# Kernel optimization log

Measured on AMD Instinct MI355X. Metric: run time of the kernel, lower is better.

Reference implementation:

```python
import jax, jax.numpy as jnp
import numpy as np

N = 50000      # nodes
E = 1600000    # edges (before self-loops)
H = 4          # heads
C = 32         # channels per head
HC = H * C     # hidden_channels = 128
IN = 128       # in_channels
NCLS = 4       # classifier out_channels
B = 512        # number of graphs
NEG_SLOPE = 0.2


def setup_inputs() -> dict:
    key = jax.random.key(0)
    ks = jax.random.split(key, 14)
    s = 0.1
    return {
        "x": jax.random.normal(ks[0], (N, IN), jnp.float32),
        "edge_index": jax.random.randint(ks[1], (2, E), 0, N, dtype=jnp.int32),
        "batch": jnp.sort(jax.random.randint(ks[2], (N,), 0, B, dtype=jnp.int32)),
        "w1": jax.random.normal(ks[3], (IN, HC), jnp.float32) * s,
        "as1": jax.random.normal(ks[4], (H, C), jnp.float32) * s,
        "ad1": jax.random.normal(ks[5], (H, C), jnp.float32) * s,
        "b1": jnp.zeros((HC,), jnp.float32),
        "w2": jax.random.normal(ks[6], (HC, HC), jnp.float32) * s,
        "as2": jax.random.normal(ks[7], (H, C), jnp.float32) * s,
        "ad2": jax.random.normal(ks[8], (H, C), jnp.float32) * s,
        "b2": jnp.zeros((HC,), jnp.float32),
        "wc": jax.random.normal(ks[9], (HC, NCLS), jnp.float32) * s,
        "bc": jnp.zeros((NCLS,), jnp.float32),
    }


def gat_conv(x, W, a_src, a_dst, bias, src, dst):
    # x: [N, F_in]; W: [F_in, H*C]
    h = (x @ W).reshape(N, H, C)                      # [N, H, C]
    e_src = jnp.einsum('nhc,hc->nh', h, a_src)        # [N, H]
    e_dst = jnp.einsum('nhc,hc->nh', h, a_dst)
    # per-edge attention logits, softmax grouped by destination node
    e = jax.nn.leaky_relu(e_src[src] + e_dst[dst], NEG_SLOPE)      # [E', H]
    m = jax.ops.segment_max(e, dst, num_segments=N)                # [N, H]
    m = jnp.where(jnp.isfinite(m), m, 0.0)
    ex = jnp.exp(e - jax.lax.stop_gradient(m)[dst])
    denom = jax.ops.segment_sum(ex, dst, num_segments=N)
    alpha = ex / (denom[dst] + 1e-16)                               # [E', H]
    out = jax.ops.segment_sum(alpha[:, :, None] * h[src], dst, num_segments=N)
    return out.reshape(N, HC) + bias                  # concat heads + bias


def reference(x, edge_index, batch, w1, as1, ad1, b1, w2, as2, ad2, b2, wc, bc):
    x = x.astype(jnp.float32)
    # GATConv default add_self_loops=True
    loops = jnp.arange(N, dtype=edge_index.dtype)
    src = jnp.concatenate([edge_index[0], loops])
    dst = jnp.concatenate([edge_index[1], loops])
    h = gat_conv(x, w1, as1, ad1, b1, src, dst)
    h = jax.nn.relu(h)                                # act between layers; dropout=0 (eval)
    h = gat_conv(h, w2, as2, ad2, b2, src, dst)
    # global_mean_pool over batch ids
    sums = jax.ops.segment_sum(h, batch, num_segments=B)            # [B, HC]
    cnts = jax.ops.segment_sum(jnp.ones((N,), h.dtype), batch, num_segments=B)
    pooled = sums / jnp.maximum(cnts, 1.0)[:, None]
    return pooled @ wc + bc                            # [B, NCLS]
```

## Files before the change

kernel.cpp:

```cpp
#include <hip/hip_runtime.h>
#include <hip/hip_fp16.h>

#define N_NODES 50000
#define N_EDGES 1600000
#define EPLUS   1650000
#define HCH 128
#define NB 512
#define NCLS 4
#define NBUCK 782
#define NSB 256
#define PCHUNK 6446

typedef unsigned int uint;
typedef __attribute__((ext_vector_type(8))) _Float16 f16x8;
typedef __attribute__((ext_vector_type(4))) float f32x4;

__device__ __forceinline__ float lrelu(float v) { return v > 0.f ? v : 0.2f * v; }

__device__ __forceinline__ float fdot2(uint a, uint b, float c) {
  asm("v_dot2_f32_f16 %0, %1, %2, %0" : "+v"(c) : "v"(a), "v"(b));
  return c;
}

__device__ __forceinline__ uint pkrtz(float a, float b) {
  auto v = __builtin_amdgcn_cvt_pkrtz(a, b);
  uint r;
  __builtin_memcpy(&r, &v, 4);
  return r;
}

__device__ __forceinline__ uint pkrn(float a, float b) {
  return (uint)__half_as_ushort(__float2half_rn(a)) |
         ((uint)__half_as_ushort(__float2half_rn(b)) << 16);
}

__global__ __launch_bounds__(256) void k_pA(const int* __restrict__ ei,
                                            int* __restrict__ M) {
  __shared__ int lh[NBUCK];
  for (int k = threadIdx.x; k < NBUCK; k += 256) lh[k] = 0;
  __syncthreads();
  int lo = blockIdx.x * PCHUNK;
  int hi = lo + PCHUNK; if (hi > EPLUS) hi = EPLUS;
  for (int e = lo + threadIdx.x; e < hi; e += 256) {
    int dst = (e < N_EDGES) ? ei[N_EDGES + e] : (e - N_EDGES);
    atomicAdd(&lh[dst >> 6], 1);
  }
  __syncthreads();
  for (int k = threadIdx.x; k < NBUCK; k += 256)
    M[blockIdx.x * NBUCK + k] = lh[k];
}

__global__ __launch_bounds__(256) void k_pB1(int* __restrict__ M,
                                             int* __restrict__ tot) {
  __shared__ int sm[256];
  int k = blockIdx.x;
  int t = threadIdx.x;
  int v = M[t * NBUCK + k];
  sm[t] = v;
  __syncthreads();
  for (int off = 1; off < 256; off <<= 1) {
    int u = (t >= off) ? sm[t - off] : 0;
    __syncthreads();
    sm[t] += u;
    __syncthreads();
  }
  M[t * NBUCK + k] = sm[t] - v;
  if (t == 255) tot[k] = sm[255];
}

__global__ __launch_bounds__(1024) void k_pB2(const int* __restrict__ tot,
                                              int* __restrict__ bucketstart) {
  __shared__ int sm[1024];
  int k = threadIdx.x;
  int v = (k < NBUCK) ? tot[k] : 0;
  sm[k] = v;
  __syncthreads();
  for (int off = 1; off < 1024; off <<= 1) {
    int u = (k >= off) ? sm[k - off] : 0;
    __syncthreads();
    sm[k] += u;
    __syncthreads();
  }
  if (k < NBUCK) {
    bucketstart[k] = sm[k] - v;
    if (k == NBUCK - 1) bucketstart[NBUCK] = sm[k];
  }
}

__global__ __launch_bounds__(256) void k_pC(const int* __restrict__ ei,
                                            const int* __restrict__ M,
                                            const int* __restrict__ bucketstart,
                                            uint* __restrict__ part) {
  __shared__ int lbase[NBUCK];
  __shared__ int lc[NBUCK];
  for (int k = threadIdx.x; k < NBUCK; k += 256) {
    lbase[k] = bucketstart[k] + M[blockIdx.x * NBUCK + k];
    lc[k] = 0;
  }
  __syncthreads();
  int lo = blockIdx.x * PCHUNK;
  int hi = lo + PCHUNK; if (hi > EPLUS) hi = EPLUS;
  for (int e = lo + threadIdx.x; e < hi; e += 256) {
    int src, dst;
    if (e < N_EDGES) { src = ei[e]; dst = ei[N_EDGES + e]; }
    else { src = dst = e - N_EDGES; }
    int b = dst >> 6;
    int p = lbase[b] + atomicAdd(&lc[b], 1);
    part[p] = (uint)src | ((uint)dst << 16);
  }
}

__global__ __launch_bounds__(256) void k_pD(const uint* __restrict__ part,
                                            const int* __restrict__ bucketstart,
                                            int* __restrict__ rowstart,
                                            int* __restrict__ col) {
  __shared__ int dcnt[64], dstart[64], dc2[64];
  int b = blockIdx.x;
  int n0 = bucketstart[b], n1 = bucketstart[b + 1];
  int t = threadIdx.x;
  if (t < 64) { dcnt[t] = 0; dc2[t] = 0; }
  __syncthreads();
  for (int i = n0 + t; i < n1; i += 256)
    atomicAdd(&dcnt[(part[i] >> 16) & 63], 1);
  __syncthreads();
  if (t < 64) {
    int v = dcnt[t];
    int run = v;
    #pragma unroll
    for (int off = 1; off < 64; off <<= 1) {
      int u = __shfl_up(run, off);
      if (t >= off) run += u;
    }
    dstart[t] = run - v;
    int node = b * 64 + t;
    if (node < N_NODES) rowstart[node] = n0 + run - v;
  }
  if (b == NBUCK - 1 && t == 0) rowstart[N_NODES] = n1;
  __syncthreads();
  for (int i = n0 + t; i < n1; i += 256) {
    uint pr = part[i];
    int loc = (pr >> 16) & 63;
    int pos = n0 + dstart[loc] + atomicAdd(&dc2[loc], 1);
    col[pos] = (int)(pr & 0xffffu);
  }
}

template<int XF16>
__global__ __launch_bounds__(256) void k_gemm_fused(const float* __restrict__ X,
                                                    const uint* __restrict__ X16,
                                                    const float* __restrict__ W,
                                                    const float* __restrict__ asrc,
                                                    const float* __restrict__ adst,
                                                    uint* __restrict__ hbu,
                                                    float* __restrict__ es,
                                                    float* __restrict__ ed) {
  __shared__ uint As[64][68];
  __shared__ uint Bf[32 * 256];
  int tid = threadIdx.x;
  int lane = tid & 63;
  int wv = tid >> 6;
  int r0 = blockIdx.x * 64;

  if (XF16) {
    #pragma unroll
    for (int i = 0; i < 4; ++i) {
      int q = tid + 256 * i;
      int row = q >> 4;
      int u4 = q & 15;
      int gr = r0 + row;
      uint4 v = make_uint4(0u, 0u, 0u, 0u);
      if (gr < N_NODES) v = *(const uint4*)&X16[(size_t)gr * 64 + u4 * 4];
      *(uint4*)&As[row][u4 * 4] = v;
    }
  } else {
    #pragma unroll
    for (int i = 0; i < 8; ++i) {
      int q = tid + 256 * i;
      int row = q >> 5;
      int f4 = q & 31;
      int gr = r0 + row;
      float4 v = make_float4(0.f, 0.f, 0.f, 0.f);
      if (gr < N_NODES) v = *(const float4*)&X[(size_t)gr * 128 + f4 * 4];
      As[row][f4 * 2 + 0] = pkrn(v.x, v.y);
      As[row][f4 * 2 + 1] = pkrn(v.z, v.w);
    }
  }
  #pragma unroll
  for (int i = 0; i < 8; ++i) {
    int f = wv + 4 * i;
    int t = f >> 2, kb = f & 3;
    int c = t * 16 + (lane & 15);
    int k0 = kb * 32 + (lane >> 4) * 8;
    const float* wp = &W[(size_t)k0 * 128 + c];
    uint4 b;
    b.x = pkrn(wp[0],   wp[128]);
    b.y = pkrn(wp[256], wp[384]);
    b.z = pkrn(wp[512], wp[640]);
    b.w = pkrn(wp[768], wp[896]);
    *(uint4*)&Bf[f * 256 + lane * 4] = b;
  }
  __syncthreads();

  int rb = wv * 16;
  f32x4 acc[8];
  #pragma unroll
  for (int t = 0; t < 8; ++t) acc[t] = (f32x4){0.f, 0.f, 0.f, 0.f};
  #pragma unroll
  for (int kb = 0; kb < 4; ++kb) {
    uint4 a4 = *(const uint4*)&As[rb + (lane & 15)][kb * 16 + (lane >> 4) * 4];
    f16x8 af; __builtin_memcpy(&af, &a4, 16);
    #pragma unroll
    for (int t = 0; t < 8; ++t) {
      uint4 b4 = *(const uint4*)&Bf[(t * 4 + kb) * 256 + lane * 4];
      f16x8 bfr; __builtin_memcpy(&bfr, &b4, 16);
      acc[t] = __builtin_amdgcn_mfma_f32_16x16x32_f16(af, bfr, acc[t], 0, 0, 0);
    }
  }

  float asv[8], adv[8];
  #pragma unroll
  for (int t = 0; t < 8; ++t) {
    asv[t] = asrc[t * 16 + (lane & 15)];
    adv[t] = adst[t * 16 + (lane & 15)];
  }
  #pragma unroll
  for (int j = 0; j < 4; ++j) {
    int row = r0 + rb + (lane >> 4) * 4 + j;
    float ps[4], pd[4];
    #pragma unroll
    for (int m = 0; m < 4; ++m) {
      ps[m] = fmaf(acc[2 * m][j], asv[2 * m], acc[2 * m + 1][j] * asv[2 * m + 1]);
      pd[m] = fmaf(acc[2 * m][j], adv[2 * m], acc[2 * m + 1][j] * adv[2 * m + 1]);
    }
    #pragma unroll
    for (int off = 1; off < 16; off <<= 1) {
      #pragma unroll
      for (int m = 0; m < 4; ++m) {
        ps[m] += __shfl_xor(ps[m], off);
        pd[m] += __shfl_xor(pd[m], off);
      }
    }
    #pragma unroll
    for (int t = 0; t < 8; ++t) {
      float other = __shfl_xor(acc[t][j], 1);
      if (!(lane & 1) && row < N_NODES) {
        hbu[(size_t)row * 64 + t * 8 + ((lane & 15) >> 1)] = pkrn(acc[t][j], other);
      }
    }
    if ((lane & 15) == 0 && row < N_NODES) {
      #pragma unroll
      for (int m = 0; m < 4; ++m) {
        es[row * 4 + m] = ps[m];
        ed[row * 4 + m] = pd[m];
      }
    }
  }
}

__global__ __launch_bounds__(256) void k_attn(const uint* __restrict__ hb,
                                              const float* __restrict__ es,
                                              const float* __restrict__ ed,
                                              const int* __restrict__ rowstart,
                                              const int* __restrict__ col,
                                              const float* __restrict__ bias,
                                              float* __restrict__ outp,
                                              uint* __restrict__ out16,
                                              int do_relu, int wf16) {
  __shared__ float swv[4][4 * 68];
  __shared__ int   ssc[4][64];
  int lane = threadIdx.x & 63;
  int wv = threadIdx.x >> 6;
  int n = blockIdx.x * 4 + wv;
  if (n >= N_NODES) return;
  int s = rowstart[n], t = rowstart[n + 1];
  int sub = lane & 15;
  int esel = lane >> 4;
  int head2 = sub >> 2;
  float4 edv = *(const float4*)&ed[n * 4];
  const char* hbb = (const char*)hb + (uint)sub * 16u;
  const char* esb = (const char*)es;
  float* wv0 = swv[wv];
  int* sc0 = ssc[wv];

  float4 denv = make_float4(0.f, 0.f, 0.f, 0.f);
  float acc[8];
  #pragma unroll
  for (int j = 0; j < 8; ++j) acc[j] = 0.f;

  for (int base = s; base < t; base += 64) {
    int nthis = t - base; if (nthis > 64) nthis = 64;
    int npad = (nthis + 15) & ~15;
    if (lane < nthis) {
      int sc = col[base + lane];
      float4 esv = *(const float4*)(esb + ((uint)sc << 4));
      float w0 = __expf(lrelu(esv.x + edv.x));
      float w1 = __expf(lrelu(esv.y + edv.y));
      float w2 = __expf(lrelu(esv.z + edv.z));
      float w3 = __expf(lrelu(esv.w + edv.w));
      denv.x += w0; denv.y += w1; denv.z += w2; denv.w += w3;
      wv0[0 * 68 + lane] = w0;
      wv0[1 * 68 + lane] = w1;
      wv0[2 * 68 + lane] = w2;
      wv0[3 * 68 + lane] = w3;
      sc0[lane] = sc << 8;
    } else if (lane < npad) {
      wv0[0 * 68 + lane] = 0.f;
      wv0[1 * 68 + lane] = 0.f;
      wv0[2 * 68 + lane] = 0.f;
      wv0[3 * 68 + lane] = 0.f;
      sc0[lane] = 0;
    }
    asm volatile("s_waitcnt lgkmcnt(0)" ::: "memory");
    __builtin_amdgcn_s_setprio(1);
    for (int i = 0; i < npad; i += 16) {
      int e0 = i + esel, e1 = e0 + 4, e2 = e0 + 8, e3 = e0 + 12;
      float w0 = wv0[head2 * 68 + e0];
      float w1 = wv0[head2 * 68 + e1];
      float w2 = wv0[head2 * 68 + e2];
      float w3 = wv0[head2 * 68 + e3];
      int so0 = sc0[e0], so1 = sc0[e1], so2 = sc0[e2], so3 = sc0[e3];
      uint4 q0 = *(const uint4*)(hbb + (uint)so0);
      uint4 q1 = *(const uint4*)(hbb + (uint)so1);
      uint4 q2 = *(const uint4*)(hbb + (uint)so2);
      uint4 q3 = *(const uint4*)(hbb + (uint)so3);
      uint wa = pkrtz(w0, w1);
      uint wb = pkrtz(w2, w3);
      acc[0] = fdot2(__builtin_amdgcn_perm(q1.x, q0.x, 0x05040100u), wa, acc[0]);
      acc[1] = fdot2(__builtin_amdgcn_perm(q1.x, q0.x, 0x07060302u), wa, acc[1]);
      acc[2] = fdot2(__builtin_amdgcn_perm(q1.y, q0.y, 0x05040100u), wa, acc[2]);
      acc[3] = fdot2(__builtin_amdgcn_perm(q1.y, q0.y, 0x07060302u), wa, acc[3]);
      acc[4] = fdot2(__builtin_amdgcn_perm(q1.z, q0.z, 0x05040100u), wa, acc[4]);
      acc[5] = fdot2(__builtin_amdgcn_perm(q1.z, q0.z, 0x07060302u), wa, acc[5]);
      acc[6] = fdot2(__builtin_amdgcn_perm(q1.w, q0.w, 0x05040100u), wa, acc[6]);
      acc[7] = fdot2(__builtin_amdgcn_perm(q1.w, q0.w, 0x07060302u), wa, acc[7]);
      acc[0] = fdot2(__builtin_amdgcn_perm(q3.x, q2.x, 0x05040100u), wb, acc[0]);
      acc[1] = fdot2(__builtin_amdgcn_perm(q3.x, q2.x, 0x07060302u), wb, acc[1]);
      acc[2] = fdot2(__builtin_amdgcn_perm(q3.y, q2.y, 0x05040100u), wb, acc[2]);
      acc[3] = fdot2(__builtin_amdgcn_perm(q3.y, q2.y, 0x07060302u), wb, acc[3]);
      acc[4] = fdot2(__builtin_amdgcn_perm(q3.z, q2.z, 0x05040100u), wb, acc[4]);
      acc[5] = fdot2(__builtin_amdgcn_perm(q3.z, q2.z, 0x07060302u), wb, acc[5]);
      acc[6] = fdot2(__builtin_amdgcn_perm(q3.w, q2.w, 0x05040100u), wb, acc[6]);
      acc[7] = fdot2(__builtin_amdgcn_perm(q3.w, q2.w, 0x07060302u), wb, acc[7]);
    }
    __builtin_amdgcn_s_setprio(0);
  }
  #pragma unroll
  for (int j = 0; j < 8; ++j) {
    acc[j] += __shfl_xor(acc[j], 16);
    acc[j] += __shfl_xor(acc[j], 32);
  }
  #pragma unroll
  for (int off = 1; off < 64; off <<= 1) {
    denv.x += __shfl_xor(denv.x, off);
    denv.y += __shfl_xor(denv.y, off);
    denv.z += __shfl_xor(denv.z, off);
    denv.w += __shfl_xor(denv.w, off);
  }
  float den = (head2 & 2) ? ((head2 & 1) ? denv.w : denv.z)
                          : ((head2 & 1) ? denv.y : denv.x);
  float inv = 1.0f / (den + 1e-16f);
  if (lane < 32) {
    int half = lane >> 4;
    int c = sub * 8 + half * 4;
    float4 bb = *(const float4*)&bias[c];
    float o0 = acc[half * 4 + 0] * inv + bb.x;
    float o1 = acc[half * 4 + 1] * inv + bb.y;
    float o2 = acc[half * 4 + 2] * inv + bb.z;
    float o3 = acc[half * 4 + 3] * inv + bb.w;
    if (do_relu) {
      o0 = fmaxf(o0, 0.f); o1 = fmaxf(o1, 0.f);
      o2 = fmaxf(o2, 0.f); o3 = fmaxf(o3, 0.f);
    }
    if (wf16) {
      uint2 p2;
      p2.x = pkrn(o0, o1);
      p2.y = pkrn(o2, o3);
      *(uint2*)&out16[(size_t)n * 64 + sub * 4 + half * 2] = p2;
    } else {
      *(float4*)&outp[(size_t)n * 128 + c] = make_float4(o0, o1, o2, o3);
    }
  }
}

__global__ __launch_bounds__(128) void k_poolcls(const float* __restrict__ out2,
                                                 const int* __restrict__ batch,
                                                 const float* __restrict__ wc,
                                                 const float* __restrict__ bc,
                                                 float* __restrict__ y) {
  int b = blockIdx.x;
  int c = threadIdx.x;
  int lo = 0, hi = N_NODES;
  while (lo < hi) { int mid = (lo + hi) >> 1; if (batch[mid] < b) lo = mid + 1; else hi = mid; }
  int s = lo;
  lo = s; hi = N_NODES;
  while (lo < hi) { int mid = (lo + hi) >> 1; if (batch[mid] < b + 1) lo = mid + 1; else hi = mid; }
  int e = lo;
  float acc0 = 0.f, acc1 = 0.f, acc2 = 0.f, acc3 = 0.f;
  int nidx = s;
  for (; nidx + 4 <= e; nidx += 4) {
    acc0 += out2[(size_t)nidx * 128 + c];
    acc1 += out2[(size_t)(nidx + 1) * 128 + c];
    acc2 += out2[(size_t)(nidx + 2) * 128 + c];
    acc3 += out2[(size_t)(nidx + 3) * 128 + c];
  }
  for (; nidx < e; ++nidx) acc0 += out2[(size_t)nidx * 128 + c];
  float acc = (acc0 + acc1) + (acc2 + acc3);
  float cnt = (float)(e - s);
  float pooled = acc / fmaxf(cnt, 1.0f);
  float4 wrow = *(const float4*)&wc[c * 4];
  float wj[4] = {wrow.x, wrow.y, wrow.z, wrow.w};
  __shared__ float red[128];
  #pragma unroll
  for (int j = 0; j < 4; ++j) {
    red[c] = pooled * wj[j];
    __syncthreads();
    for (int off = 64; off > 0; off >>= 1) {
      if (c < off) red[c] += red[c + off];
      __syncthreads();
    }
    if (c == 0) y[b * 4 + j] = red[0] + bc[j];
    __syncthreads();
  }
}

extern "C" void kernel_launch(void* const* d_in, const int* in_sizes, int n_in,
                              void* d_out, int out_size, void* d_ws, size_t ws_size,
                              hipStream_t stream) {
  const float* x    = (const float*)d_in[0];
  const int*   ei   = (const int*)d_in[1];
  const int*   batch= (const int*)d_in[2];
  const float* w1   = (const float*)d_in[3];
  const float* as1  = (const float*)d_in[4];
  const float* ad1  = (const float*)d_in[5];
  const float* b1   = (const float*)d_in[6];
  const float* w2   = (const float*)d_in[7];
  const float* as2  = (const float*)d_in[8];
  const float* ad2  = (const float*)d_in[9];
  const float* b2   = (const float*)d_in[10];
  const float* wc   = (const float*)d_in[11];
  const float* bc   = (const float*)d_in[12];
  float* y = (float*)d_out;

  char* ws = (char*)d_ws;
  size_t o = 0;
  auto take = [&](size_t bytes) { void* p = ws + o; o = (o + bytes + 255) & ~(size_t)255; return p; };
  uint*  hbu      = (uint*)take((size_t)N_NODES * 64 * 4);
  uint*  h1u      = (uint*)take((size_t)N_NODES * 64 * 4);
  float* obuf     = (float*)take((size_t)N_NODES * HCH * 4);
  float* es       = (float*)take((size_t)N_NODES * 4 * 4);
  float* ed       = (float*)take((size_t)N_NODES * 4 * 4);
  int*   M        = (int*)take((size_t)NSB * NBUCK * 4);
  int*   tot      = (int*)take((size_t)NBUCK * 4);
  int*   bstart   = (int*)take((size_t)(NBUCK + 1) * 4);
  uint*  part     = (uint*)take((size_t)EPLUS * 4);
  int*   rowstart = (int*)take((size_t)(N_NODES + 1) * 4);
  int*   col      = (int*)take((size_t)EPLUS * 4);

  const int GW = N_NODES / 4;
  const int GG = (N_NODES + 63) / 64;

  k_pA<<<NSB, 256, 0, stream>>>(ei, M);
  k_pB1<<<NBUCK, 256, 0, stream>>>(M, tot);
  k_pB2<<<1, 1024, 0, stream>>>(tot, bstart);
  k_pC<<<NSB, 256, 0, stream>>>(ei, M, bstart, part);
  k_pD<<<NBUCK, 256, 0, stream>>>(part, bstart, rowstart, col);

  k_gemm_fused<0><<<GG, 256, 0, stream>>>(x, nullptr, w1, as1, ad1, hbu, es, ed);
  k_attn<<<GW, 256, 0, stream>>>(hbu, es, ed, rowstart, col, b1, obuf, h1u, 1, 1);

  k_gemm_fused<1><<<GG, 256, 0, stream>>>(nullptr, h1u, w2, as2, ad2, hbu, es, ed);
  k_attn<<<GW, 256, 0, stream>>>(hbu, es, ed, rowstart, col, b2, obuf, h1u, 0, 0);

  k_poolcls<<<NB, 128, 0, stream>>>(obuf, batch, wc, bc, y);
}
```

Before: 218.8 us.

## Merge CSR finalize and first-layer GEMM into one interleaved launch

```diff
diff --git a/kernel.cpp b/kernel.cpp
--- a/kernel.cpp
+++ b/kernel.cpp
@@ -110,44 +110,143 @@
   }
 }
 
-__global__ __launch_bounds__(256) void k_pD(const uint* __restrict__ part,
-                                            const int* __restrict__ bucketstart,
-                                            int* __restrict__ rowstart,
-                                            int* __restrict__ col) {
-  __shared__ int dcnt[64], dstart[64], dc2[64];
-  int b = blockIdx.x;
-  int n0 = bucketstart[b], n1 = bucketstart[b + 1];
-  int t = threadIdx.x;
-  if (t < 64) { dcnt[t] = 0; dc2[t] = 0; }
-  __syncthreads();
-  for (int i = n0 + t; i < n1; i += 256)
-    atomicAdd(&dcnt[(part[i] >> 16) & 63], 1);
-  __syncthreads();
-  if (t < 64) {
-    int v = dcnt[t];
-    int run = v;
-    #pragma unroll
-    for (int off = 1; off < 64; off <<= 1) {
-      int u = __shfl_up(run, off);
-      if (t >= off) run += u;
-    }
-    dstart[t] = run - v;
-    int node = b * 64 + t;
-    if (node < N_NODES) rowstart[node] = n0 + run - v;
-  }
-  if (b == NBUCK - 1 && t == 0) rowstart[N_NODES] = n1;
-  __syncthreads();
-  for (int i = n0 + t; i < n1; i += 256) {
-    uint pr = part[i];
-    int loc = (pr >> 16) & 63;
-    int pos = n0 + dstart[loc] + atomicAdd(&dc2[loc], 1);
-    col[pos] = (int)(pr & 0xffffu);
-  }
-}
-
-template<int XF16>
-__global__ __launch_bounds__(256) void k_gemm_fused(const float* __restrict__ X,
-                                                    const uint* __restrict__ X16,
+__global__ __launch_bounds__(256) void k_pD_gemm(const uint* __restrict__ part,
+                                                 const int* __restrict__ bucketstart,
+                                                 int* __restrict__ rowstart,
+                                                 int* __restrict__ col,
+                                                 const float* __restrict__ X,
+                                                 const float* __restrict__ W,
+                                                 const float* __restrict__ asrc,
+                                                 const float* __restrict__ adst,
+                                                 uint* __restrict__ hbu,
+                                                 float* __restrict__ es,
+                                                 float* __restrict__ ed) {
+  __shared__ char smem[50176];
+  int tid = threadIdx.x;
+  if (blockIdx.x & 1) {
+    int* dcnt   = (int*)smem;
+    int* dstart = dcnt + 64;
+    int* dc2    = dstart + 64;
+    int b = blockIdx.x >> 1;
+    int n0 = bucketstart[b], n1 = bucketstart[b + 1];
+    int t = tid;
+    if (t < 64) { dcnt[t] = 0; dc2[t] = 0; }
+    __syncthreads();
+    for (int i = n0 + t; i < n1; i += 256)
+      atomicAdd(&dcnt[(part[i] >> 16) & 63], 1);
+    __syncthreads();
+    if (t < 64) {
+      int v = dcnt[t];
+      int run = v;
+      #pragma unroll
+      for (int off = 1; off < 64; off <<= 1) {
+        int u = __shfl_up(run, off);
+        if (t >= off) run += u;
+      }
+      dstart[t] = run - v;
+      int node = b * 64 + t;
+      if (node < N_NODES) rowstart[node] = n0 + run - v;
+    }
+    if (b == NBUCK - 1 && t == 0) rowstart[N_NODES] = n1;
+    __syncthreads();
+    for (int i = n0 + t; i < n1; i += 256) {
+      uint pr = part[i];
+      int loc = (pr >> 16) & 63;
+      int pos = n0 + dstart[loc] + atomicAdd(&dc2[loc], 1);
+      col[pos] = (int)((pr & 0xffffu) << 8);
+    }
+  } else {
+    uint (*As)[68] = (uint(*)[68])smem;
+    uint* Bf = (uint*)(smem + 17408);
+    int lane = tid & 63;
+    int wv = tid >> 6;
+    int r0 = (blockIdx.x >> 1) * 64;
+
+    #pragma unroll
+    for (int i = 0; i < 8; ++i) {
+      int q = tid + 256 * i;
+      int row = q >> 5;
+      int f4 = q & 31;
+      int gr = r0 + row;
+      float4 v = make_float4(0.f, 0.f, 0.f, 0.f);
+      if (gr < N_NODES) v = *(const float4*)&X[(size_t)gr * 128 + f4 * 4];
+      As[row][f4 * 2 + 0] = pkrn(v.x, v.y);
+      As[row][f4 * 2 + 1] = pkrn(v.z, v.w);
+    }
+    #pragma unroll
+    for (int i = 0; i < 8; ++i) {
+      int f = wv + 4 * i;
+      int t = f >> 2, kb = f & 3;
+      int c = t * 16 + (lane & 15);
+      int k0 = kb * 32 + (lane >> 4) * 8;
+      const float* wp = &W[(size_t)k0 * 128 + c];
+      uint4 b;
+      b.x = pkrn(wp[0],   wp[128]);
+      b.y = pkrn(wp[256], wp[384]);
+      b.z = pkrn(wp[512], wp[640]);
+      b.w = pkrn(wp[768], wp[896]);
+      *(uint4*)&Bf[f * 256 + lane * 4] = b;
+    }
+    __syncthreads();
+
+    int rb = wv * 16;
+    f32x4 acc[8];
+    #pragma unroll
+    for (int t = 0; t < 8; ++t) acc[t] = (f32x4){0.f, 0.f, 0.f, 0.f};
+    #pragma unroll
+    for (int kb = 0; kb < 4; ++kb) {
+      uint4 a4 = *(const uint4*)&As[rb + (lane & 15)][kb * 16 + (lane >> 4) * 4];
+      f16x8 af; __builtin_memcpy(&af, &a4, 16);
+      #pragma unroll
+      for (int t = 0; t < 8; ++t) {
+        uint4 b4 = *(const uint4*)&Bf[(t * 4 + kb) * 256 + lane * 4];
+        f16x8 bfr; __builtin_memcpy(&bfr, &b4, 16);
+        acc[t] = __builtin_amdgcn_mfma_f32_16x16x32_f16(af, bfr, acc[t], 0, 0, 0);
+      }
+    }
+
+    float asv[8], adv[8];
+    #pragma unroll
+    for (int t = 0; t < 8; ++t) {
+      asv[t] = asrc[t * 16 + (lane & 15)];
+      adv[t] = adst[t * 16 + (lane & 15)];
+    }
+    #pragma unroll
+    for (int j = 0; j < 4; ++j) {
+      int row = r0 + rb + (lane >> 4) * 4 + j;
+      float ps[4], pd[4];
+      #pragma unroll
+      for (int m = 0; m < 4; ++m) {
+        ps[m] = fmaf(acc[2 * m][j], asv[2 * m], acc[2 * m + 1][j] * asv[2 * m + 1]);
+        pd[m] = fmaf(acc[2 * m][j], adv[2 * m], acc[2 * m + 1][j] * adv[2 * m + 1]);
+      }
+      #pragma unroll
+      for (int off = 1; off < 16; off <<= 1) {
+        #pragma unroll
+        for (int m = 0; m < 4; ++m) {
+          ps[m] += __shfl_xor(ps[m], off);
+          pd[m] += __shfl_xor(pd[m], off);
+        }
+      }
+      #pragma unroll
+      for (int t = 0; t < 8; ++t) {
+        float other = __shfl_xor(acc[t][j], 1);
+        if (!(lane & 1) && row < N_NODES) {
+          hbu[(size_t)row * 64 + t * 8 + ((lane & 15) >> 1)] = pkrn(acc[t][j], other);
+        }
+      }
+      if ((lane & 15) == 0 && row < N_NODES) {
+        #pragma unroll
+        for (int m = 0; m < 4; ++m) {
+          es[row * 4 + m] = ps[m];
+          ed[row * 4 + m] = pd[m];
+        }
+      }
+    }
+  }
+}
+
+__global__ __launch_bounds__(256) void k_gemm_fused(const uint* __restrict__ X16,
                                                     const float* __restrict__ W,
                                                     const float* __restrict__ asrc,
                                                     const float* __restrict__ adst,
@@ -161,29 +260,15 @@
   int wv = tid >> 6;
   int r0 = blockIdx.x * 64;
 
-  if (XF16) {
-    #pragma unroll
-    for (int i = 0; i < 4; ++i) {
-      int q = tid + 256 * i;
-      int row = q >> 4;
-      int u4 = q & 15;
-      int gr = r0 + row;
-      uint4 v = make_uint4(0u, 0u, 0u, 0u);
-      if (gr < N_NODES) v = *(const uint4*)&X16[(size_t)gr * 64 + u4 * 4];
-      *(uint4*)&As[row][u4 * 4] = v;
-    }
-  } else {
-    #pragma unroll
-    for (int i = 0; i < 8; ++i) {
-      int q = tid + 256 * i;
-      int row = q >> 5;
-      int f4 = q & 31;
-      int gr = r0 + row;
-      float4 v = make_float4(0.f, 0.f, 0.f, 0.f);
-      if (gr < N_NODES) v = *(const float4*)&X[(size_t)gr * 128 + f4 * 4];
-      As[row][f4 * 2 + 0] = pkrn(v.x, v.y);
-      As[row][f4 * 2 + 1] = pkrn(v.z, v.w);
-    }
+  #pragma unroll
+  for (int i = 0; i < 4; ++i) {
+    int q = tid + 256 * i;
+    int row = q >> 4;
+    int u4 = q & 15;
+    int gr = r0 + row;
+    uint4 v = make_uint4(0u, 0u, 0u, 0u);
+    if (gr < N_NODES) v = *(const uint4*)&X16[(size_t)gr * 64 + u4 * 4];
+    *(uint4*)&As[row][u4 * 4] = v;
   }
   #pragma unroll
   for (int i = 0; i < 8; ++i) {
@@ -291,8 +376,8 @@
     int nthis = t - base; if (nthis > 64) nthis = 64;
     int npad = (nthis + 15) & ~15;
     if (lane < nthis) {
-      int sc = col[base + lane];
-      float4 esv = *(const float4*)(esb + ((uint)sc << 4));
+      int so = col[base + lane];
+      float4 esv = *(const float4*)(esb + ((uint)so >> 4));
       float w0 = __expf(lrelu(esv.x + edv.x));
       float w1 = __expf(lrelu(esv.y + edv.y));
       float w2 = __expf(lrelu(esv.z + edv.z));
@@ -302,7 +387,7 @@
       wv0[1 * 68 + lane] = w1;
       wv0[2 * 68 + lane] = w2;
       wv0[3 * 68 + lane] = w3;
-      sc0[lane] = sc << 8;
+      sc0[lane] = so;
     } else if (lane < npad) {
       wv0[0 * 68 + lane] = 0.f;
       wv0[1 * 68 + lane] = 0.f;
@@ -463,12 +548,13 @@
   k_pB1<<<NBUCK, 256, 0, stream>>>(M, tot);
   k_pB2<<<1, 1024, 0, stream>>>(tot, bstart);
   k_pC<<<NSB, 256, 0, stream>>>(ei, M, bstart, part);
-  k_pD<<<NBUCK, 256, 0, stream>>>(part, bstart, rowstart, col);
-
-  k_gemm_fused<0><<<GG, 256, 0, stream>>>(x, nullptr, w1, as1, ad1, hbu, es, ed);
+
+  k_pD_gemm<<<2 * GG, 256, 0, stream>>>(part, bstart, rowstart, col,
+                                        x, w1, as1, ad1, hbu, es, ed);
+
   k_attn<<<GW, 256, 0, stream>>>(hbu, es, ed, rowstart, col, b1, obuf, h1u, 1, 1);
 
-  k_gemm_fused<1><<<GG, 256, 0, stream>>>(nullptr, h1u, w2, as2, ad2, hbu, es, ed);
+  k_gemm_fused<<<GG, 256, 0, stream>>>(h1u, w2, as2, ad2, hbu, es, ed);
   k_attn<<<GW, 256, 0, stream>>>(hbu, es, ed, rowstart, col, b2, obuf, h1u, 0, 0);
 
   k_poolcls<<<NB, 128, 0, stream>>>(obuf, batch, wc, bc, y);
```

Result: no change. 216.3 us (-1.1%).
